# Kernel tuning notes

Hardware: AMD Instinct MI355X
Metric: run time of the kernel (lower is better)

Reference implementation:

```python
import jax, jax.numpy as jnp
import numpy as np

B, N, H, E = 8, 256, 128, 32

def setup_inputs() -> dict:
    key = jax.random.key(0)
    ks = jax.random.split(key, 9)
    x = jax.random.normal(ks[0], (B, N, H), dtype=jnp.float32)
    adj = jax.random.randint(ks[1], (B, N, N), 0, 2, dtype=jnp.int32)
    e = jax.random.normal(ks[2], (B, N, N, E), dtype=jnp.float32)
    s = 0.02
    We = jax.random.normal(ks[3], (E, H), dtype=jnp.float32) * s
    be = jax.random.normal(ks[4], (H,), dtype=jnp.float32) * s
    W1 = jax.random.normal(ks[5], (H, 2 * H), dtype=jnp.float32) * s
    b1 = jax.random.normal(ks[6], (2 * H,), dtype=jnp.float32) * s
    W2 = jax.random.normal(ks[7], (2 * H, H), dtype=jnp.float32) * s
    b2 = jax.random.normal(ks[8], (H,), dtype=jnp.float32) * s
    return {"x": x, "adj": adj, "e": e, "We": We, "be": be,
            "W1": W1, "b1": b1, "W2": W2, "b2": b2}

def reference(x, adj, e, We, be, W1, b1, W2, b2):
    # edge projection: [B,N,N,E] -> [B,N,N,H]
    e_h = jnp.einsum('bije,eh->bijh', e, We) + be
    # message m[b,i,j] = relu(x[b,j] + e_h[b,i,j]); mask by adj
    m = jax.nn.relu(x[:, None, :, :] + e_h)
    m = jnp.where((adj != 0)[..., None], m, jnp.zeros((), m.dtype))
    agg = m.sum(axis=2)  # sum over j -> [B,N,H]
    h = agg + x
    out = jax.nn.relu(h @ W1 + b1) @ W2 + b2
    return out
```

## Files before the change

kernel.cpp:

```cpp
#include <hip/hip_runtime.h>
#include <hip/hip_bf16.h>

#define B_ 8
#define N_ 256
#define H_ 128
#define E_ 32
#define XLS_STRIDE 264

typedef __bf16 bf16x8 __attribute__((ext_vector_type(8)));
typedef __bf16 bf16x4 __attribute__((ext_vector_type(4)));
typedef float f32x4 __attribute__((ext_vector_type(4)));

static __device__ __forceinline__ __bf16 f2bf(float f) {
    union { float f; unsigned int u; } a;
    a.f = f;
    const unsigned int r = a.u + 0x7FFFu + ((a.u >> 16) & 1u);
    union { unsigned short s; __bf16 b; } o;
    o.s = (unsigned short)(r >> 16);
    return o.b;
}

#define W1T_OFF  131072
#define W2T_OFF  163840
#define WEBF_OFF 196608

__global__ __launch_bounds__(256) void prep_kernel(
    const float* __restrict__ x, const float* __restrict__ be,
    const float* __restrict__ W1, const float* __restrict__ W2,
    const float* __restrict__ We, float* __restrict__ ws)
{
    const int blk = blockIdx.x;
    if (blk == 320) {
        __bf16* Webf = (__bf16*)(ws + WEBF_OFF);
        for (int q = threadIdx.x; q < 512; q += 256) {
            const int quad = q >> 7, h = q & 127;
            bf16x8 t;
#pragma unroll
            for (int kk = 0; kk < 8; ++kk)
                t[kk] = f2bf(We[(quad * 8 + kk) * H_ + h]);
            *(bf16x8*)&Webf[q * 8] = t;
        }
        return;
    }
    __shared__ float tile[32][33];
    const int tx = threadIdx.x & 31, ty = threadIdx.x >> 5;
    if (blk < 256) {
        const int b = blk >> 5, t = blk & 31;
        const float* src = x + (size_t)b * N_ * H_;
        __bf16* dst = (__bf16*)ws + (size_t)b * H_ * N_;
        const int r0 = (t >> 2) * 32, c0 = (t & 3) * 32;
#pragma unroll
        for (int p = 0; p < 4; ++p)
            tile[ty + p * 8][tx] =
                src[(size_t)(r0 + ty + p * 8) * H_ + c0 + tx] + be[c0 + tx];
        __syncthreads();
#pragma unroll
        for (int p = 0; p < 4; ++p)
            dst[(size_t)(c0 + ty + p * 8) * N_ + r0 + tx] = f2bf(tile[tx][ty + p * 8]);
        return;
    }
    const float* src; float* dst; int R, C, r0, c0;
    if (blk < 288) {
        const int t = blk - 256;
        src = W1; dst = ws + W1T_OFF;
        R = 128; C = 256; r0 = (t >> 3) * 32; c0 = (t & 7) * 32;
    } else {
        const int t = blk - 288;
        src = W2; dst = ws + W2T_OFF;
        R = 256; C = 128; r0 = (t >> 2) * 32; c0 = (t & 3) * 32;
    }
#pragma unroll
    for (int p = 0; p < 4; ++p)
        tile[ty + p * 8][tx] = src[(size_t)(r0 + ty + p * 8) * C + c0 + tx];
    __syncthreads();
#pragma unroll
    for (int p = 0; p < 4; ++p)
        dst[(size_t)(c0 + ty + p * 8) * R + r0 + tx] = tile[tx][ty + p * 8];
}

__global__ __launch_bounds__(256, 2) void agg_kernel(
    const int* __restrict__ adj, const float* __restrict__ e,
    const float* __restrict__ ws, const float* __restrict__ x,
    float* __restrict__ hout)
{
    __shared__ __bf16 xls[H_ * XLS_STRIDE];
    __shared__ float red[4][128];
    const int bi   = blockIdx.x;
    const int b    = bi >> 8;
    const int tid  = threadIdx.x;
    const int w    = tid >> 6;
    const int lane = tid & 63;
    const int quad = lane >> 4;
    const int col  = lane & 15;

    const size_t ebase   = (size_t)bi * (N_ * E_);
    const size_t adjbase = (size_t)bi * N_;

    float4 a0v[2], a1v[2];
    int4   avv[2];
#pragma unroll
    for (int p = 0; p < 2; ++p) {
        const int j0 = (p * 4 + w) * 16;
        const float* ap = e + ebase + (size_t)(j0 + col) * E_ + quad * 8;
        a0v[p] = *(const float4*)ap;
        a1v[p] = *(const float4*)(ap + 4);
        avv[p] = *(const int4*)(adj + adjbase + j0 + quad * 4);
    }

    {
        const __bf16* gx = (const __bf16*)ws + (size_t)b * (H_ * N_);
#pragma unroll 4
        for (int it = 0; it < 16; ++it) {
            const int k   = it * 256 + tid;
            const int row = k >> 5, cc = k & 31;
            const f32x4 v = *(const f32x4*)(gx + (size_t)row * 256 + cc * 8);
            *(f32x4*)&xls[row * XLS_STRIDE + cc * 8] = v;
        }
    }

    const __bf16* Webf = (const __bf16*)(ws + WEBF_OFF);
    bf16x8 bw[8];
#pragma unroll
    for (int ht = 0; ht < 8; ++ht)
        bw[ht] = *(const bf16x8*)&Webf[(quad * 128 + ht * 16 + col) * 8];

    float psum[8];
#pragma unroll
    for (int ht = 0; ht < 8; ++ht) psum[ht] = 0.0f;

    const f32x4 zero4 = {0.0f, 0.0f, 0.0f, 0.0f};

    __syncthreads();

#pragma unroll
    for (int c = 0; c < 4; ++c) {
        const int s  = c & 1;
        const int jr = (c * 4 + w) * 16 + quad * 4;

        bf16x8 af;
        af[0] = f2bf(a0v[s].x); af[1] = f2bf(a0v[s].y);
        af[2] = f2bf(a0v[s].z); af[3] = f2bf(a0v[s].w);
        af[4] = f2bf(a1v[s].x); af[5] = f2bf(a1v[s].y);
        af[6] = f2bf(a1v[s].z); af[7] = f2bf(a1v[s].w);
        float adjf[4];
        adjf[0] = avv[s].x ? 1.0f : 0.0f;
        adjf[1] = avv[s].y ? 1.0f : 0.0f;
        adjf[2] = avv[s].z ? 1.0f : 0.0f;
        adjf[3] = avv[s].w ? 1.0f : 0.0f;

        if (c < 2) {
            const int j0n = ((c + 2) * 4 + w) * 16;
            const float* apn = e + ebase + (size_t)(j0n + col) * E_ + quad * 8;
            a0v[s] = *(const float4*)apn;
            a1v[s] = *(const float4*)(apn + 4);
            avv[s] = *(const int4*)(adj + adjbase + j0n + quad * 4);
        }

#pragma unroll
        for (int g = 0; g < 2; ++g) {
            f32x4 acc[4];
#pragma unroll
            for (int t = 0; t < 4; ++t)
                acc[t] = __builtin_amdgcn_mfma_f32_16x16x32_bf16(af, bw[g * 4 + t], zero4, 0, 0, 0);
#pragma unroll
            for (int t = 0; t < 4; ++t) {
                const int ht = g * 4 + t;
                const bf16x4 xv = *(const bf16x4*)&xls[(ht * 16 + col) * XLS_STRIDE + jr];
#pragma unroll
                for (int r = 0; r < 4; ++r)
                    psum[ht] += adjf[r] * fmaxf(acc[t][r] + (float)xv[r], 0.0f);
            }
        }
    }

#pragma unroll
    for (int ht = 0; ht < 8; ++ht) {
        float v = psum[ht];
        v += __shfl_xor(v, 16);
        v += __shfl_xor(v, 32);
        if (lane < 16) red[w][ht * 16 + lane] = v;
    }
    __syncthreads();
    if (tid < 128) {
        const float aggv = red[0][tid] + red[1][tid] + red[2][tid] + red[3][tid];
        hout[(size_t)bi * H_ + tid] = aggv + x[(size_t)bi * H_ + tid];
    }
}

__global__ __launch_bounds__(256) void mlp_kernel(
    const float* __restrict__ ws, const float* __restrict__ b1,
    const float* __restrict__ b2, float* __restrict__ hio)
{
    __shared__ float hs[8][128];
    __shared__ float ts[8][256];
    __shared__ float part[8][2][128];
    const int tid = threadIdx.x;
    const int r0  = blockIdx.x * 8;

    ((f32x4*)hs)[tid] = ((const f32x4*)(hio + (size_t)r0 * H_))[tid];
    __syncthreads();

    {
        const float* wrow = ws + W1T_OFF + (size_t)tid * 128;
        float acc[8] = {0.f, 0.f, 0.f, 0.f, 0.f, 0.f, 0.f, 0.f};
        for (int k = 0; k < 128; k += 4) {
            const f32x4 wv = *(const f32x4*)&wrow[k];
#pragma unroll
            for (int r = 0; r < 8; ++r) {
                const f32x4 hv = *(const f32x4*)&hs[r][k];
                acc[r] += hv[0] * wv[0] + hv[1] * wv[1] + hv[2] * wv[2] + hv[3] * wv[3];
            }
        }
        const float bb = b1[tid];
#pragma unroll
        for (int r = 0; r < 8; ++r) ts[r][tid] = fmaxf(acc[r] + bb, 0.0f);
    }
    __syncthreads();

    {
        const int c  = tid & 127;
        const int kb = (tid >> 7) * 128;
        const float* wrow = ws + W2T_OFF + (size_t)c * 256 + kb;
        float acc[8] = {0.f, 0.f, 0.f, 0.f, 0.f, 0.f, 0.f, 0.f};
        for (int k = 0; k < 128; k += 4) {
            const f32x4 wv = *(const f32x4*)&wrow[k];
#pragma unroll
            for (int r = 0; r < 8; ++r) {
                const f32x4 tv = *(const f32x4*)&ts[r][kb + k];
                acc[r] += tv[0] * wv[0] + tv[1] * wv[1] + tv[2] * wv[2] + tv[3] * wv[3];
            }
        }
#pragma unroll
        for (int r = 0; r < 8; ++r) part[r][tid >> 7][c] = acc[r];
    }
    __syncthreads();
#pragma unroll
    for (int idx = tid; idx < 1024; idx += 256) {
        const int r = idx >> 7, c = idx & 127;
        hio[(size_t)(r0 + r) * H_ + c] = part[r][0][c] + part[r][1][c] + b2[c];
    }
}

extern "C" void kernel_launch(void* const* d_in, const int* in_sizes, int n_in,
                              void* d_out, int out_size, void* d_ws, size_t ws_size,
                              hipStream_t stream) {
    const float* x   = (const float*)d_in[0];
    const int*   adj = (const int*)  d_in[1];
    const float* e   = (const float*)d_in[2];
    const float* We  = (const float*)d_in[3];
    const float* be  = (const float*)d_in[4];
    const float* W1  = (const float*)d_in[5];
    const float* b1  = (const float*)d_in[6];
    const float* W2  = (const float*)d_in[7];
    const float* b2  = (const float*)d_in[8];
    float* out = (float*)d_out;
    float* ws  = (float*)d_ws;

    prep_kernel<<<dim3(321), dim3(256), 0, stream>>>(x, be, W1, W2, We, ws);
    agg_kernel<<<dim3(B_ * N_), dim3(256), 0, stream>>>(adj, e, ws, x, out);
    mlp_kernel<<<dim3(B_ * N_ / 8), dim3(256), 0, stream>>>(ws, b1, b2, out);
}
```

Baseline: 141.3 us.

## Split agg kernel across hidden halves to cut LDS and raise occupancy

Each aggregation block now handles 64 of the 128 hidden features, with twice as many blocks launched. This halves the shared-memory x tile and the per-thread accumulators, so more blocks can fit per CU (launch bound raised to 3). Loads of the x tile from LDS are also hoisted before the MFMAs. The trade-off is that each block of edge features and the adjacency are read twice, relying on L2 reuse between paired blocks.

```diff
diff --git a/kernel.cpp b/kernel.cpp
--- a/kernel.cpp
+++ b/kernel.cpp
@@ -78,14 +78,15 @@
         dst[(size_t)(c0 + ty + p * 8) * R + r0 + tx] = tile[tx][ty + p * 8];
 }
 
-__global__ __launch_bounds__(256, 2) void agg_kernel(
+__global__ __launch_bounds__(256, 3) void agg_kernel(
     const int* __restrict__ adj, const float* __restrict__ e,
     const float* __restrict__ ws, const float* __restrict__ x,
     float* __restrict__ hout)
 {
-    __shared__ __bf16 xls[H_ * XLS_STRIDE];
-    __shared__ float red[4][128];
-    const int bi   = blockIdx.x;
+    __shared__ __bf16 xls[64 * XLS_STRIDE];
+    __shared__ float red[4][64];
+    const int bi   = blockIdx.x >> 1;
+    const int hh   = blockIdx.x & 1;
     const int b    = bi >> 8;
     const int tid  = threadIdx.x;
     const int w    = tid >> 6;
@@ -108,9 +109,10 @@
     }
 
     {
-        const __bf16* gx = (const __bf16*)ws + (size_t)b * (H_ * N_);
-#pragma unroll 4
-        for (int it = 0; it < 16; ++it) {
+        const __bf16* gx = (const __bf16*)ws + (size_t)b * (H_ * N_)
+                         + (size_t)(hh * 64) * N_;
+#pragma unroll
+        for (int it = 0; it < 8; ++it) {
             const int k   = it * 256 + tid;
             const int row = k >> 5, cc = k & 31;
             const f32x4 v = *(const f32x4*)(gx + (size_t)row * 256 + cc * 8);
@@ -119,14 +121,14 @@
     }
 
     const __bf16* Webf = (const __bf16*)(ws + WEBF_OFF);
-    bf16x8 bw[8];
-#pragma unroll
-    for (int ht = 0; ht < 8; ++ht)
-        bw[ht] = *(const bf16x8*)&Webf[(quad * 128 + ht * 16 + col) * 8];
-
-    float psum[8];
-#pragma unroll
-    for (int ht = 0; ht < 8; ++ht) psum[ht] = 0.0f;
+    bf16x8 bw[4];
+#pragma unroll
+    for (int t = 0; t < 4; ++t)
+        bw[t] = *(const bf16x8*)&Webf[(quad * 128 + hh * 64 + t * 16 + col) * 8];
+
+    float psum[4];
+#pragma unroll
+    for (int t = 0; t < 4; ++t) psum[t] = 0.0f;
 
     const f32x4 zero4 = {0.0f, 0.0f, 0.0f, 0.0f};
 
@@ -136,6 +138,11 @@
     for (int c = 0; c < 4; ++c) {
         const int s  = c & 1;
         const int jr = (c * 4 + w) * 16 + quad * 4;
+
+        bf16x4 xv[4];
+#pragma unroll
+        for (int t = 0; t < 4; ++t)
+            xv[t] = *(const bf16x4*)&xls[(t * 16 + col) * XLS_STRIDE + jr];
 
         bf16x8 af;
         af[0] = f2bf(a0v[s].x); af[1] = f2bf(a0v[s].y);
@@ -156,34 +163,29 @@
             avv[s] = *(const int4*)(adj + adjbase + j0n + quad * 4);
         }
 
-#pragma unroll
-        for (int g = 0; g < 2; ++g) {
-            f32x4 acc[4];
-#pragma unroll
-            for (int t = 0; t < 4; ++t)
-                acc[t] = __builtin_amdgcn_mfma_f32_16x16x32_bf16(af, bw[g * 4 + t], zero4, 0, 0, 0);
-#pragma unroll
-            for (int t = 0; t < 4; ++t) {
-                const int ht = g * 4 + t;
-                const bf16x4 xv = *(const bf16x4*)&xls[(ht * 16 + col) * XLS_STRIDE + jr];
-#pragma unroll
-                for (int r = 0; r < 4; ++r)
-                    psum[ht] += adjf[r] * fmaxf(acc[t][r] + (float)xv[r], 0.0f);
-            }
-        }
-    }
-
-#pragma unroll
-    for (int ht = 0; ht < 8; ++ht) {
-        float v = psum[ht];
+        f32x4 acc[4];
+#pragma unroll
+        for (int t = 0; t < 4; ++t)
+            acc[t] = __builtin_amdgcn_mfma_f32_16x16x32_bf16(af, bw[t], zero4, 0, 0, 0);
+#pragma unroll
+        for (int t = 0; t < 4; ++t)
+#pragma unroll
+            for (int r = 0; r < 4; ++r)
+                psum[t] += adjf[r] * fmaxf(acc[t][r] + (float)xv[t][r], 0.0f);
+    }
+
+#pragma unroll
+    for (int t = 0; t < 4; ++t) {
+        float v = psum[t];
         v += __shfl_xor(v, 16);
         v += __shfl_xor(v, 32);
-        if (lane < 16) red[w][ht * 16 + lane] = v;
-    }
-    __syncthreads();
-    if (tid < 128) {
+        if (lane < 16) red[w][t * 16 + lane] = v;
+    }
+    __syncthreads();
+    if (tid < 64) {
+        const int hofs = hh * 64 + tid;
         const float aggv = red[0][tid] + red[1][tid] + red[2][tid] + red[3][tid];
-        hout[(size_t)bi * H_ + tid] = aggv + x[(size_t)bi * H_ + tid];
+        hout[(size_t)bi * H_ + hofs] = aggv + x[(size_t)bi * H_ + hofs];
     }
 }
 
@@ -257,6 +259,6 @@
     float* ws  = (float*)d_ws;
 
     prep_kernel<<<dim3(321), dim3(256), 0, stream>>>(x, be, W1, W2, We, ws);
-    agg_kernel<<<dim3(B_ * N_), dim3(256), 0, stream>>>(adj, e, ws, x, out);
+    agg_kernel<<<dim3(B_ * N_ * 2), dim3(256), 0, stream>>>(adj, e, ws, x, out);
     mlp_kernel<<<dim3(B_ * N_ / 8), dim3(256), 0, stream>>>(ws, b1, b2, out);
 }
```

Measured after the change: 143.1 us. About the same (+1.3%).
